# Performance work log

Measured on AMD Instinct MI355X. Metric: run time of the kernel, lower is better.

Reference implementation:

```python
import jax, jax.numpy as jnp
import numpy as np

TEMP = 0.07
W00 = 0.1
EPS = 1e-8


def setup_inputs() -> dict:
    key = jax.random.key(0)
    k1, k2, k3, k4 = jax.random.split(key, 4)
    B, N, D = 32, 256, 256
    M = B * N
    return {
        "audio_feats": jax.random.normal(k1, (B, N, D), dtype=jnp.float32),
        "visual_feats": jax.random.normal(k2, (B, N, D), dtype=jnp.float32),
        "audio_labels": jax.random.randint(k3, (M,), 0, 2, dtype=jnp.int64)
            if jax.config.jax_enable_x64 else jax.random.randint(k3, (M,), 0, 2, dtype=jnp.int32),
        "visual_labels": jax.random.randint(k4, (M,), 0, 2, dtype=jnp.int64)
            if jax.config.jax_enable_x64 else jax.random.randint(k4, (M,), 0, 2, dtype=jnp.int32),
    }


def reference(audio_feats, visual_feats, audio_labels, visual_labels):
    B, N, D = audio_feats.shape
    M = B * N
    a = audio_feats.reshape(M, D)
    v = visual_feats.reshape(M, D)
    # L2 normalize (torch F.normalize uses eps=1e-12 clamp on norm)
    a = a / jnp.maximum(jnp.linalg.norm(a, axis=-1, keepdims=True), 1e-12)
    v = v / jnp.maximum(jnp.linalg.norm(v, axis=-1, keepdims=True), 1e-12)
    sim = (a @ v.T) / TEMP  # (M, M)
    exp_sim = jnp.exp(sim)
    la = audio_labels[:, None]  # (M, 1)
    lv = visual_labels[None, :]  # (1, M)
    pos_mask = (la == lv) & ((la == 1) | (la == 0))
    weight = jnp.where(la == 1, 1.0, W00) * pos_mask.astype(sim.dtype)  # (M, M)
    wexp = exp_sim * weight

    # audio -> visual (row direction)
    denom_a2v = exp_sim.sum(axis=1)
    num_a2v = wexp.sum(axis=1)
    frac_a2v = (num_a2v + EPS) / (denom_a2v + EPS)
    valid_a2v = (num_a2v > 0).astype(sim.dtype)
    loss_a2v = -(valid_a2v * jnp.log(frac_a2v)).sum() / jnp.maximum(valid_a2v.sum(), 1.0)

    # visual -> audio (column direction)
    denom_v2a = exp_sim.sum(axis=0)
    num_v2a = wexp.sum(axis=0)
    frac_v2a = (num_v2a + EPS) / (denom_v2a + EPS)
    valid_v2a = (num_v2a > 0).astype(sim.dtype)
    loss_v2a = -(valid_v2a * jnp.log(frac_v2a)).sum() / jnp.maximum(valid_v2a.sum(), 1.0)

    return 0.5 * (loss_a2v + loss_v2a)
```

## Files before the change

### kernel.cpp

```cpp
#include <hip/hip_runtime.h>

#define M_ROWS 8192
#define D_DIM  256
#define BM     128
#define BN     128
#define NBI    (M_ROWS / BM)
#define NBJ    (M_ROWS / BN)
#define NJOBS  (NBI * NBJ)

#define ALPHA  4.53982478f


typedef __attribute__((ext_vector_type(4))) float  floatx4;

__device__ inline unsigned short f2bf(float f) {
    union { float f; unsigned int u; } v; v.f = f;
    unsigned int u = v.u;
    u = (u + 0x7fffu + ((u >> 16) & 1u)) >> 16;
    return (unsigned short)u;
}

__device__ inline float bf2f(unsigned short b) {
    union { unsigned int u; float f; } v; v.u = (unsigned int)b << 16;
    return v.f;
}

__device__ inline float fast_exp2(float x) {
#if __has_builtin(__builtin_amdgcn_exp2f)
    return __builtin_amdgcn_exp2f(x);
#else
    return exp2f(x);
#endif
}

__global__ __launch_bounds__(256) void normalize_kernel(
    const float* __restrict__ af, const float* __restrict__ vf,
    unsigned char* __restrict__ aB, unsigned char* __restrict__ vB,
    float* __restrict__ glob)
{
    __shared__ unsigned short tileS[16 * 264];

    if (blockIdx.x == 0) {
        if (threadIdx.x < 4) glob[threadIdx.x] = 0.f;
        if (threadIdx.x == 4) ((int*)glob)[4] = 0;
    }

    const int b = blockIdx.x;
    const bool isA = b < 512;
    const int T = isA ? b : b - 512;
    const float* src = (isA ? af : vf) + (size_t)T * 16 * D_DIM;
    unsigned char* dst = (isA ? aB : vB) + (size_t)T * 4096;

    const int t = threadIdx.x;
    const int row = t >> 4, c = t & 15;

    const float* p = src + row * D_DIM + c * 16;
    float4 x0 = ((const float4*)p)[0], x1 = ((const float4*)p)[1];
    float4 x2 = ((const float4*)p)[2], x3 = ((const float4*)p)[3];
    float ss = x0.x*x0.x + x0.y*x0.y + x0.z*x0.z + x0.w*x0.w
             + x1.x*x1.x + x1.y*x1.y + x1.z*x1.z + x1.w*x1.w
             + x2.x*x2.x + x2.y*x2.y + x2.z*x2.z + x2.w*x2.w
             + x3.x*x3.x + x3.y*x3.y + x3.z*x3.z + x3.w*x3.w;
    #pragma unroll
    for (int m = 1; m < 16; m <<= 1) ss += __shfl_xor(ss, m, 64);
    float scale = ALPHA / fmaxf(sqrtf(ss), 1e-12f);

    unsigned short* q = tileS + row * 264 + c * 16;
    ushort4 o0, o1, o2, o3;
    o0.x = f2bf(x0.x*scale); o0.y = f2bf(x0.y*scale); o0.z = f2bf(x0.z*scale); o0.w = f2bf(x0.w*scale);
    o1.x = f2bf(x1.x*scale); o1.y = f2bf(x1.y*scale); o1.z = f2bf(x1.z*scale); o1.w = f2bf(x1.w*scale);
    o2.x = f2bf(x2.x*scale); o2.y = f2bf(x2.y*scale); o2.z = f2bf(x2.z*scale); o2.w = f2bf(x2.w*scale);
    o3.x = f2bf(x3.x*scale); o3.y = f2bf(x3.y*scale); o3.z = f2bf(x3.z*scale); o3.w = f2bf(x3.w*scale);
    ((ushort4*)q)[0] = o0; ((ushort4*)q)[1] = o1;
    ((ushort4*)q)[2] = o2; ((ushort4*)q)[3] = o3;
    __syncthreads();

    #pragma unroll
    for (int s = 0; s < 2; ++s) {
        const int ch  = t + s * 256;
        const int l16 = ch & 15, quad = (ch >> 4) & 3, k32 = ch >> 6;
        const unsigned short* rp = &tileS[l16 * 264 + k32 * 32 + quad * 8];
        float f0 = bf2f(rp[0]), f1 = bf2f(rp[1]), f2 = bf2f(rp[2]), f3 = bf2f(rp[3]);
        float f4 = bf2f(rp[4]), f5 = bf2f(rp[5]), f6 = bf2f(rp[6]), f7 = bf2f(rp[7]);
        int p0 = __builtin_amdgcn_cvt_pk_fp8_f32(f0, f1, 0, false);
        p0     = __builtin_amdgcn_cvt_pk_fp8_f32(f2, f3, p0, true);
        int p1 = __builtin_amdgcn_cvt_pk_fp8_f32(f4, f5, 0, false);
        p1     = __builtin_amdgcn_cvt_pk_fp8_f32(f6, f7, p1, true);
        int2 outv; outv.x = p0; outv.y = p1;
        *(int2*)(dst + (size_t)ch * 8) = outv;
    }
}

__global__ __launch_bounds__(256, 3) void gemm_loss_kernel(
    const unsigned char* __restrict__ aB, const unsigned char* __restrict__ vB,
    const int* __restrict__ la, const int* __restrict__ lv,
    float* __restrict__ rowPart, float* __restrict__ colPart)
{
    const int tid  = threadIdx.x;
    const int wave = tid >> 6, lane = tid & 63;
    const int quad = lane >> 4, l16 = lane & 15;

    const int super = blockIdx.x >> 8;
    const int inner = blockIdx.x & 255;
    const int bx = (super & 3) * 16 + (inner & 15);
    const int by = (super >> 2) * 16 + (inner >> 4);
    const int i0 = bx * BM, j0 = by * BN;

    const unsigned char* Abase = aB + ((size_t)(bx * 8 + wave * 2) * 512 + lane) * 8;
    const unsigned char* Vbase = vB + ((size_t)(by * 8) * 512 + lane) * 8;

    floatx4 acc[2][8] = {};
    long long afr[3][2], bfr[3][8];

    #pragma unroll
    for (int s = 0; s < 2; ++s) {
        #pragma unroll
        for (int it = 0; it < 2; ++it)
            afr[s][it] = *(const long long*)(Abase + it * 4096 + s * 512);
        #pragma unroll
        for (int jt = 0; jt < 8; ++jt)
            bfr[s][jt] = *(const long long*)(Vbase + jt * 4096 + s * 512);
    }

    #pragma unroll
    for (int k32 = 0; k32 < 8; ++k32) {
        const int cur = k32 % 3;
        if (k32 < 6) {
            const int nx = (k32 + 2) % 3;
            const size_t ko = (size_t)(k32 + 2) * 512;
            #pragma unroll
            for (int it = 0; it < 2; ++it)
                afr[nx][it] = *(const long long*)(Abase + it * 4096 + ko);
            #pragma unroll
            for (int jt = 0; jt < 8; ++jt)
                bfr[nx][jt] = *(const long long*)(Vbase + jt * 4096 + ko);
        }
        #pragma unroll
        for (int it = 0; it < 2; ++it)
            #pragma unroll
            for (int jt = 0; jt < 8; ++jt)
                acc[it][jt] = __builtin_amdgcn_mfma_f32_16x16x32_fp8_fp8(
                    afr[cur][it], bfr[cur][jt], acc[it][jt], 0, 0, 0);
    }

    const int baseRow = i0 + wave * 32;
    float maf[2][4];
    #pragma unroll
    for (int it = 0; it < 2; ++it)
        #pragma unroll
        for (int r = 0; r < 4; ++r)
            maf[it][r] = (float)la[baseRow + it * 16 + quad * 4 + r];
    float mvf[8];
    #pragma unroll
    for (int jt = 0; jt < 8; ++jt)
        mvf[jt] = (float)lv[j0 + jt * 16 + l16];

    float rT[2][4] = {}, r1[2][4] = {};
    float cT[8] = {}, c1[8] = {};
    #pragma unroll
    for (int it = 0; it < 2; ++it) {
        #pragma unroll
        for (int jt = 0; jt < 8; ++jt) {
            #pragma unroll
            for (int r = 0; r < 4; ++r) {
                float e = fast_exp2(acc[it][jt][r]);
                rT[it][r] += e;
                r1[it][r] = fmaf(mvf[jt], e, r1[it][r]);
                cT[jt] += e;
                c1[jt] = fmaf(maf[it][r], e, c1[jt]);
            }
        }
    }

    #pragma unroll
    for (int jt = 0; jt < 8; ++jt) {
        float t0 = cT[jt], t1 = c1[jt];
        t0 += __shfl_xor(t0, 16, 64); t0 += __shfl_xor(t0, 32, 64);
        t1 += __shfl_xor(t1, 16, 64); t1 += __shfl_xor(t1, 32, 64);
        cT[jt] = t0; c1[jt] = t1;
    }

    __shared__ float rowbuf[2 * BM];
    __shared__ float colbuf[8 * BN];

    #pragma unroll
    for (int it = 0; it < 2; ++it) {
        #pragma unroll
        for (int r = 0; r < 4; ++r) {
            float s0 = rT[it][r], s1 = r1[it][r];
            #pragma unroll
            for (int m = 1; m < 16; m <<= 1) {
                s0 += __shfl_xor(s0, m, 64);
                s1 += __shfl_xor(s1, m, 64);
            }
            if (l16 == 0) {
                int rl = wave * 32 + it * 16 + quad * 4 + r;
                rowbuf[rl * 2 + 0] = s0;
                rowbuf[rl * 2 + 1] = s1;
            }
        }
    }
    if (quad == 0) {
        #pragma unroll
        for (int jt = 0; jt < 8; ++jt) {
            colbuf[(wave * 2 + 0) * BN + jt * 16 + l16] = cT[jt];
            colbuf[(wave * 2 + 1) * BN + jt * 16 + l16] = c1[jt];
        }
    }
    __syncthreads();

    {
        const int rl  = tid >> 1;
        const int cls = tid & 1;
        rowPart[((size_t)by * M_ROWS + i0 + rl) * 2 + cls] = rowbuf[rl * 2 + cls];
        float s = colbuf[(0 * 2 + cls) * BN + rl] + colbuf[(1 * 2 + cls) * BN + rl]
                + colbuf[(2 * 2 + cls) * BN + rl] + colbuf[(3 * 2 + cls) * BN + rl];
        colPart[((size_t)bx * M_ROWS + j0 + rl) * 2 + cls] = s;
    }
}

__global__ __launch_bounds__(256) void reduce_kernel(
    const float* __restrict__ rowPart, const float* __restrict__ colPart,
    const int* __restrict__ la, const int* __restrict__ lv,
    float* __restrict__ glob, float* __restrict__ out)
{
    const int bid = blockIdx.x;
    const bool aside = bid < 32;
    const int idx = (aside ? bid : bid - 32) * 256 + threadIdx.x;
    const float* part = aside ? rowPart : colPart;
    const int* lab = aside ? la : lv;

    float tot = 0.f, c1 = 0.f;
    #pragma unroll 4
    for (int b = 0; b < 64; ++b) {
        float2 p = *(const float2*)(part + ((size_t)b * M_ROWS + idx) * 2);
        tot += p.x; c1 += p.y;
    }
    float num = lab[idx] ? c1 : 0.1f * (tot - c1);
    float lg = 0.f, cnt = 0.f;
    if (num > 0.f) { lg = logf((num + 1e-8f) / (tot + 1e-8f)); cnt = 1.f; }

    #pragma unroll
    for (int m = 1; m < 64; m <<= 1) {
        lg  += __shfl_xor(lg,  m, 64);
        cnt += __shfl_xor(cnt, m, 64);
    }
    __shared__ float red[4][2];
    const int w = threadIdx.x >> 6, ln = threadIdx.x & 63;
    if (ln == 0) { red[w][0] = lg; red[w][1] = cnt; }
    __syncthreads();
    if (threadIdx.x == 0) {
        float slg  = red[0][0] + red[1][0] + red[2][0] + red[3][0];
        float scnt = red[0][1] + red[1][1] + red[2][1] + red[3][1];
        float* base = glob + (aside ? 0 : 2);
        atomicAdd(&base[0], slg);
        atomicAdd(&base[1], scnt);
        __threadfence();
        int old = atomicAdd((int*)glob + 4, 1);
        if (old == 63) {
            __threadfence();
            float sA = atomicAdd(&glob[0], 0.f);
            float cA = atomicAdd(&glob[1], 0.f);
            float sV = atomicAdd(&glob[2], 0.f);
            float cV = atomicAdd(&glob[3], 0.f);
            float lossA = -sA / fmaxf(cA, 1.f);
            float lossV = -sV / fmaxf(cV, 1.f);
            out[0] = 0.5f * (lossA + lossV);
        }
    }
}

extern "C" void kernel_launch(void* const* d_in, const int* in_sizes, int n_in,
                              void* d_out, int out_size, void* d_ws, size_t ws_size,
                              hipStream_t stream)
{
    const float* af = (const float*)d_in[0];
    const float* vf = (const float*)d_in[1];
    const int*   la = (const int*)d_in[2];
    const int*   lv = (const int*)d_in[3];
    float* out = (float*)d_out;

    char* ws = (char*)d_ws;
    unsigned char* aB = (unsigned char*)ws;
    unsigned char* vB = (unsigned char*)(ws + 2ull * 1024 * 1024);
    float* rowPart   = (float*)(ws +  4ull * 1024 * 1024);
    float* colPart   = (float*)(ws +  8ull * 1024 * 1024);
    float* glob      = (float*)(ws + 12ull * 1024 * 1024);

    normalize_kernel<<<1024, 256, 0, stream>>>(af, vf, aB, vB, glob);
    gemm_loss_kernel<<<NJOBS, 256, 0, stream>>>(aB, vB, la, lv, rowPart, colPart);
    reduce_kernel<<<64, 256, 0, stream>>>(rowPart, colPart, la, lv, glob, out);
}
```

Baseline: 130.4 us.

## Give each wave an independent 64x128 tile and fuse reduction into GEMM tail

Each wave now computes its own 64x128 tile in two 32-row passes with double-buffered fragment loads, writing row and column partials straight to global memory. This removes the block-level shared-memory exchange and __syncthreads, at the cost of twice as many column partials and less V-fragment reuse across waves. The final 64 blocks to finish, found with a global atomic counter, spin-wait until all blocks are done and then perform the reduction, replacing the separate reduce kernel launch. The spin-wait assumes those last blocks are resident together with the rest, which holds only because they are the last to arrive.

```diff
diff --git a/kernel.cpp b/kernel.cpp
--- a/kernel.cpp
+++ b/kernel.cpp
@@ -2,11 +2,8 @@
 
 #define M_ROWS 8192
 #define D_DIM  256
-#define BM     128
-#define BN     128
-#define NBI    (M_ROWS / BM)
-#define NBJ    (M_ROWS / BN)
-#define NJOBS  (NBI * NBJ)
+#define TOTB   2048
+#define NRED   64
 
 #define ALPHA  4.53982478f
 
@@ -42,7 +39,7 @@
 
     if (blockIdx.x == 0) {
         if (threadIdx.x < 4) glob[threadIdx.x] = 0.f;
-        if (threadIdx.x == 4) ((int*)glob)[4] = 0;
+        if (threadIdx.x >= 4 && threadIdx.x < 7) ((int*)glob)[threadIdx.x] = 0;
     }
 
     const int b = blockIdx.x;
@@ -94,80 +91,97 @@
 __global__ __launch_bounds__(256, 3) void gemm_loss_kernel(
     const unsigned char* __restrict__ aB, const unsigned char* __restrict__ vB,
     const int* __restrict__ la, const int* __restrict__ lv,
-    float* __restrict__ rowPart, float* __restrict__ colPart)
+    float* __restrict__ rowPart, float* __restrict__ colPart,
+    float* __restrict__ glob, float* __restrict__ out)
 {
     const int tid  = threadIdx.x;
     const int wave = tid >> 6, lane = tid & 63;
     const int quad = lane >> 4, l16 = lane & 15;
 
-    const int super = blockIdx.x >> 8;
-    const int inner = blockIdx.x & 255;
-    const int bx = (super & 3) * 16 + (inner & 15);
-    const int by = (super >> 2) * 16 + (inner >> 4);
-    const int i0 = bx * BM, j0 = by * BN;
-
-    const unsigned char* Abase = aB + ((size_t)(bx * 8 + wave * 2) * 512 + lane) * 8;
+    const int job  = blockIdx.x * 4 + wave;
+    const int by   = job >> 7;
+    const int bx64 = job & 127;
+    const int i0 = bx64 * 64, j0 = by * 128;
+
+    const unsigned char* Abase = aB + ((size_t)(bx64 * 4) * 512 + lane) * 8;
     const unsigned char* Vbase = vB + ((size_t)(by * 8) * 512 + lane) * 8;
 
-    floatx4 acc[2][8] = {};
-    long long afr[3][2], bfr[3][8];
-
-    #pragma unroll
-    for (int s = 0; s < 2; ++s) {
-        #pragma unroll
-        for (int it = 0; it < 2; ++it)
-            afr[s][it] = *(const long long*)(Abase + it * 4096 + s * 512);
-        #pragma unroll
-        for (int jt = 0; jt < 8; ++jt)
-            bfr[s][jt] = *(const long long*)(Vbase + jt * 4096 + s * 512);
-    }
-
-    #pragma unroll
-    for (int k32 = 0; k32 < 8; ++k32) {
-        const int cur = k32 % 3;
-        if (k32 < 6) {
-            const int nx = (k32 + 2) % 3;
-            const size_t ko = (size_t)(k32 + 2) * 512;
-            #pragma unroll
-            for (int it = 0; it < 2; ++it)
-                afr[nx][it] = *(const long long*)(Abase + it * 4096 + ko);
-            #pragma unroll
-            for (int jt = 0; jt < 8; ++jt)
-                bfr[nx][jt] = *(const long long*)(Vbase + jt * 4096 + ko);
-        }
-        #pragma unroll
-        for (int it = 0; it < 2; ++it)
-            #pragma unroll
-            for (int jt = 0; jt < 8; ++jt)
-                acc[it][jt] = __builtin_amdgcn_mfma_f32_16x16x32_fp8_fp8(
-                    afr[cur][it], bfr[cur][jt], acc[it][jt], 0, 0, 0);
-    }
-
-    const int baseRow = i0 + wave * 32;
-    float maf[2][4];
-    #pragma unroll
-    for (int it = 0; it < 2; ++it)
-        #pragma unroll
-        for (int r = 0; r < 4; ++r)
-            maf[it][r] = (float)la[baseRow + it * 16 + quad * 4 + r];
     float mvf[8];
     #pragma unroll
     for (int jt = 0; jt < 8; ++jt)
         mvf[jt] = (float)lv[j0 + jt * 16 + l16];
 
-    float rT[2][4] = {}, r1[2][4] = {};
     float cT[8] = {}, c1[8] = {};
-    #pragma unroll
-    for (int it = 0; it < 2; ++it) {
-        #pragma unroll
-        for (int jt = 0; jt < 8; ++jt) {
+
+    #pragma unroll
+    for (int pass = 0; pass < 2; ++pass) {
+        const unsigned char* Ap = Abase + (size_t)pass * 2 * 4096;
+        floatx4 acc[2][8] = {};
+        long long afr[2][2], bfr[2][8];
+
+        #pragma unroll
+        for (int it = 0; it < 2; ++it) afr[0][it] = *(const long long*)(Ap + it * 4096);
+        #pragma unroll
+        for (int jt = 0; jt < 8; ++jt) bfr[0][jt] = *(const long long*)(Vbase + jt * 4096);
+
+        #pragma unroll
+        for (int k32 = 0; k32 < 8; ++k32) {
+            const int cur = k32 & 1, nxt = cur ^ 1;
+            if (k32 < 7) {
+                const size_t ko = (size_t)(k32 + 1) * 512;
+                #pragma unroll
+                for (int it = 0; it < 2; ++it)
+                    afr[nxt][it] = *(const long long*)(Ap + it * 4096 + ko);
+                #pragma unroll
+                for (int jt = 0; jt < 8; ++jt)
+                    bfr[nxt][jt] = *(const long long*)(Vbase + jt * 4096 + ko);
+            }
+            #pragma unroll
+            for (int it = 0; it < 2; ++it)
+                #pragma unroll
+                for (int jt = 0; jt < 8; ++jt)
+                    acc[it][jt] = __builtin_amdgcn_mfma_f32_16x16x32_fp8_fp8(
+                        afr[cur][it], bfr[cur][jt], acc[it][jt], 0, 0, 0);
+        }
+
+        float maf[2][4];
+        #pragma unroll
+        for (int it = 0; it < 2; ++it)
+            #pragma unroll
+            for (int r = 0; r < 4; ++r)
+                maf[it][r] = (float)la[i0 + pass * 32 + it * 16 + quad * 4 + r];
+
+        float rT[2][4] = {}, r1[2][4] = {};
+        #pragma unroll
+        for (int it = 0; it < 2; ++it) {
+            #pragma unroll
+            for (int jt = 0; jt < 8; ++jt) {
+                #pragma unroll
+                for (int r = 0; r < 4; ++r) {
+                    float e = fast_exp2(acc[it][jt][r]);
+                    rT[it][r] += e;
+                    r1[it][r] = fmaf(mvf[jt], e, r1[it][r]);
+                    cT[jt] += e;
+                    c1[jt] = fmaf(maf[it][r], e, c1[jt]);
+                }
+            }
+        }
+
+        #pragma unroll
+        for (int it = 0; it < 2; ++it) {
             #pragma unroll
             for (int r = 0; r < 4; ++r) {
-                float e = fast_exp2(acc[it][jt][r]);
-                rT[it][r] += e;
-                r1[it][r] = fmaf(mvf[jt], e, r1[it][r]);
-                cT[jt] += e;
-                c1[jt] = fmaf(maf[it][r], e, c1[jt]);
+                float s0 = rT[it][r], s1 = r1[it][r];
+                #pragma unroll
+                for (int m = 1; m < 16; m <<= 1) {
+                    s0 += __shfl_xor(s0, m, 64);
+                    s1 += __shfl_xor(s1, m, 64);
+                }
+                if (l16 == 0) {
+                    int rowg = i0 + pass * 32 + it * 16 + quad * 4 + r;
+                    float2 v2; v2.x = s0; v2.y = s1;
+                    *(float2*)&rowPart[((size_t)by * M_ROWS + rowg) * 2] = v2;
+                }
             }
         }
     }
@@ -177,66 +191,48 @@
         float t0 = cT[jt], t1 = c1[jt];
         t0 += __shfl_xor(t0, 16, 64); t0 += __shfl_xor(t0, 32, 64);
         t1 += __shfl_xor(t1, 16, 64); t1 += __shfl_xor(t1, 32, 64);
-        cT[jt] = t0; c1[jt] = t1;
-    }
-
-    __shared__ float rowbuf[2 * BM];
-    __shared__ float colbuf[8 * BN];
-
-    #pragma unroll
-    for (int it = 0; it < 2; ++it) {
-        #pragma unroll
-        for (int r = 0; r < 4; ++r) {
-            float s0 = rT[it][r], s1 = r1[it][r];
-            #pragma unroll
-            for (int m = 1; m < 16; m <<= 1) {
-                s0 += __shfl_xor(s0, m, 64);
-                s1 += __shfl_xor(s1, m, 64);
-            }
-            if (l16 == 0) {
-                int rl = wave * 32 + it * 16 + quad * 4 + r;
-                rowbuf[rl * 2 + 0] = s0;
-                rowbuf[rl * 2 + 1] = s1;
-            }
-        }
-    }
-    if (quad == 0) {
-        #pragma unroll
-        for (int jt = 0; jt < 8; ++jt) {
-            colbuf[(wave * 2 + 0) * BN + jt * 16 + l16] = cT[jt];
-            colbuf[(wave * 2 + 1) * BN + jt * 16 + l16] = c1[jt];
-        }
-    }
-    __syncthreads();
-
-    {
-        const int rl  = tid >> 1;
-        const int cls = tid & 1;
-        rowPart[((size_t)by * M_ROWS + i0 + rl) * 2 + cls] = rowbuf[rl * 2 + cls];
-        float s = colbuf[(0 * 2 + cls) * BN + rl] + colbuf[(1 * 2 + cls) * BN + rl]
-                + colbuf[(2 * 2 + cls) * BN + rl] + colbuf[(3 * 2 + cls) * BN + rl];
-        colPart[((size_t)bx * M_ROWS + j0 + rl) * 2 + cls] = s;
-    }
-}
-
-__global__ __launch_bounds__(256) void reduce_kernel(
-    const float* __restrict__ rowPart, const float* __restrict__ colPart,
-    const int* __restrict__ la, const int* __restrict__ lv,
-    float* __restrict__ glob, float* __restrict__ out)
-{
-    const int bid = blockIdx.x;
-    const bool aside = bid < 32;
-    const int idx = (aside ? bid : bid - 32) * 256 + threadIdx.x;
+        if (quad == 0) {
+            float2 v2; v2.x = t0; v2.y = t1;
+            *(float2*)&colPart[((size_t)bx64 * M_ROWS + j0 + jt * 16 + l16) * 2] = v2;
+        }
+    }
+
+    __shared__ int sRank;
+    __shared__ float red[4][2];
+    __syncthreads();
+    if (tid == 0) {
+        __threadfence();
+        int old = atomicAdd((int*)glob + 4, 1);
+        sRank = old - (TOTB - NRED);
+        if (old == TOTB - 1) {
+            __threadfence();
+            __hip_atomic_store((int*)glob + 5, 1, __ATOMIC_RELEASE, __HIP_MEMORY_SCOPE_AGENT);
+        }
+    }
+    __syncthreads();
+    const int rank = sRank;
+    if (rank < 0) return;
+
+    if (tid == 0 && rank != NRED - 1) {
+        while (__hip_atomic_load((int*)glob + 5, __ATOMIC_ACQUIRE, __HIP_MEMORY_SCOPE_AGENT) == 0)
+            __builtin_amdgcn_s_sleep(2);
+    }
+    __syncthreads();
+    __threadfence();
+
+    const bool aside = rank < 32;
+    const int idx = (aside ? rank : rank - 32) * 256 + tid;
     const float* part = aside ? rowPart : colPart;
     const int* lab = aside ? la : lv;
-
-    float tot = 0.f, c1 = 0.f;
+    const int nb = aside ? 64 : 128;
+
+    float tot = 0.f, cc1 = 0.f;
     #pragma unroll 4
-    for (int b = 0; b < 64; ++b) {
+    for (int b = 0; b < nb; ++b) {
         float2 p = *(const float2*)(part + ((size_t)b * M_ROWS + idx) * 2);
-        tot += p.x; c1 += p.y;
-    }
-    float num = lab[idx] ? c1 : 0.1f * (tot - c1);
+        tot += p.x; cc1 += p.y;
+    }
+    float num = lab[idx] ? cc1 : 0.1f * (tot - cc1);
     float lg = 0.f, cnt = 0.f;
     if (num > 0.f) { lg = logf((num + 1e-8f) / (tot + 1e-8f)); cnt = 1.f; }
 
@@ -245,19 +241,17 @@
         lg  += __shfl_xor(lg,  m, 64);
         cnt += __shfl_xor(cnt, m, 64);
     }
-    __shared__ float red[4][2];
-    const int w = threadIdx.x >> 6, ln = threadIdx.x & 63;
-    if (ln == 0) { red[w][0] = lg; red[w][1] = cnt; }
-    __syncthreads();
-    if (threadIdx.x == 0) {
+    if (lane == 0) { red[wave][0] = lg; red[wave][1] = cnt; }
+    __syncthreads();
+    if (tid == 0) {
         float slg  = red[0][0] + red[1][0] + red[2][0] + red[3][0];
         float scnt = red[0][1] + red[1][1] + red[2][1] + red[3][1];
         float* base = glob + (aside ? 0 : 2);
         atomicAdd(&base[0], slg);
         atomicAdd(&base[1], scnt);
         __threadfence();
-        int old = atomicAdd((int*)glob + 4, 1);
-        if (old == 63) {
+        int old2 = atomicAdd((int*)glob + 6, 1);
+        if (old2 == NRED - 1) {
             __threadfence();
             float sA = atomicAdd(&glob[0], 0.f);
             float cA = atomicAdd(&glob[1], 0.f);
@@ -285,9 +279,8 @@
     unsigned char* vB = (unsigned char*)(ws + 2ull * 1024 * 1024);
     float* rowPart   = (float*)(ws +  4ull * 1024 * 1024);
     float* colPart   = (float*)(ws +  8ull * 1024 * 1024);
-    float* glob      = (float*)(ws + 12ull * 1024 * 1024);
+    float* glob      = (float*)(ws + 16ull * 1024 * 1024);
 
     normalize_kernel<<<1024, 256, 0, stream>>>(af, vf, aB, vB, glob);
-    gemm_loss_kernel<<<NJOBS, 256, 0, stream>>>(aB, vB, la, lv, rowPart, colPart);
-    reduce_kernel<<<64, 256, 0, stream>>>(rowPart, colPart, la, lv, glob, out);
-}
+    gemm_loss_kernel<<<TOTB, 256, 0, stream>>>(aB, vB, la, lv, rowPart, colPart, glob, out);
+}
```

Result: slower. 318.9 us (+144.6%).
